# Kernel optimization log

Measured on AMD Instinct MI355X. Metric: run time of the kernel, lower is better.

## Reference

```python
import jax, jax.numpy as jnp
import numpy as np

N_DET, N_T, NY, NX, B = 128, 2048, 256, 256, 4


def setup_inputs() -> dict:
    key = jax.random.key(0)
    k1, k2, k3 = jax.random.split(key, 3)
    sino = jax.random.normal(k1, (B, 1, N_DET, N_T), dtype=jnp.float32)
    # lut[..., 0]: fractional time-of-flight index in [0, n_t-1)
    tof = jax.random.uniform(k2, (NY, NX, N_DET), dtype=jnp.float32) * (N_T - 1)
    # lut[..., 1]: linear-interp fraction alpha in [0, 1)
    alpha = jax.random.uniform(k3, (NY, NX, N_DET), dtype=jnp.float32)
    lut = jnp.stack([tof, alpha], axis=-1)  # [ny, nx, n_det, 2]
    return {"sino": sino, "lut": lut}


def reference(sino, lut):
    b, _, n_det, n_t = sino.shape
    ny, nx = lut.shape[0], lut.shape[1]
    P = ny * nx

    # Precompute (as in __init__): floor index, validity mask, interp fraction.
    k_floor = jnp.floor(lut[..., 0])
    valid = (k_floor >= 0) & (k_floor < n_t - 1)
    k0 = jnp.clip(k_floor, 0, max(n_t - 2, 0)).astype(jnp.int32)  # [ny,nx,n_det]
    alpha = lut[..., 1]

    # Hann apodization window over detectors (non-trainable buffer).
    apod = (0.5 - 0.5 * jnp.cos(
        2.0 * jnp.pi * jnp.arange(n_det, dtype=jnp.float32) / max(n_det - 1, 1)
    )).astype(sino.dtype)

    S = sino[:, 0]  # [B, n_det, n_t]

    # Move detector axis first so we can gather all detectors at once.
    k0t = k0.reshape(P, n_det).T          # [n_det, P]
    at = alpha.reshape(P, n_det).T        # [n_det, P]
    vt = valid.reshape(P, n_det).T.astype(sino.dtype)  # [n_det, P]

    s0 = jnp.take_along_axis(S, k0t[None], axis=2)        # [B, n_det, P]
    s1 = jnp.take_along_axis(S, (k0t + 1)[None], axis=2)  # [B, n_det, P]
    sk = ((1.0 - at) * s0 + at * s1) * vt                  # masked lerp

    out = jnp.einsum('d,bdp->bp', apod, sk)                # apodized reduce over detectors
    norm = jnp.maximum(apod.sum(), jnp.finfo(apod.dtype).tiny)
    return (out / norm).reshape(b, 1, ny, nx)
```

## Files before the change

### kernel.cpp

```cpp
#include <hip/hip_runtime.h>
#include <hip/hip_fp16.h>

#define N_DET 128
#define N_T   2048
#define NPIX  65536
#define NBATCH 4
#define G 8
#define PT 1024
#define NGB (N_DET / G)

typedef float f4_t __attribute__((ext_vector_type(4)));

__global__ __launch_bounds__(256) void sino_pack_kernel(
    const float* __restrict__ sino, float2* __restrict__ ws,
    float* __restrict__ out) {
  const int idx = blockIdx.x * blockDim.x + threadIdx.x;
  const __half2 lo = __floats2half2_rn(
      __builtin_nontemporal_load(sino + 0 * N_DET * N_T + idx),
      __builtin_nontemporal_load(sino + 1 * N_DET * N_T + idx));
  const __half2 hi = __floats2half2_rn(
      __builtin_nontemporal_load(sino + 2 * N_DET * N_T + idx),
      __builtin_nontemporal_load(sino + 3 * N_DET * N_T + idx));
  union { struct { __half2 a, b; } h; float2 f; } u;
  u.h.a = lo;
  u.h.b = hi;
  ws[idx] = u.f;
  out[idx] = 0.0f;
}

__global__ __launch_bounds__(1024, 4) void das_lds_kernel(
    const float* __restrict__ lut, const float2* __restrict__ ws,
    float* __restrict__ out) {
  __shared__ float2 sino_s[G * N_T];

  const int tid = threadIdx.x;
  const int tile = blockIdx.x;
  const int g = blockIdx.y;
  const int p = tile * PT + tid;

  f4_t l[4];
  {
    const f4_t* lp =
        reinterpret_cast<const f4_t*>(lut + ((size_t)p * N_DET + g * G) * 2);
#pragma unroll
    for (int j = 0; j < 4; ++j) l[j] = lp[j];
  }

  {
    const float4* src = reinterpret_cast<const float4*>(ws + (size_t)g * G * N_T);
    float4* dst = reinterpret_cast<float4*>(sino_s);
#pragma unroll
    for (int i = 0; i < 8192 / PT; ++i) dst[tid + i * PT] = src[tid + i * PT];
  }

  float apd[G];
#pragma unroll
  for (int j = 0; j < G; ++j) {
    apd[j] = 0.5f - 0.5f * cosf(6.28318530717958647692f *
                                ((float)(g * G + j) / (float)(N_DET - 1)));
  }
  __syncthreads();

  float a0 = 0.f, a1 = 0.f, a2 = 0.f, a3 = 0.f;
#pragma unroll
  for (int j = 0; j < G; ++j) {
    const float tof = (j & 1) ? l[j >> 1].z : l[j >> 1].x;
    const float al  = (j & 1) ? l[j >> 1].w : l[j >> 1].y;
    const float kf = floorf(tof);
    const bool valid = (kf >= 0.0f) && (kf < (float)(N_T - 1));
    const float kcl = fminf(fmaxf(kf, 0.0f), (float)(N_T - 2));
    const int k0 = (int)kcl;
    const float w = valid ? apd[j] : 0.0f;

    const float2 r0 = sino_s[j * N_T + k0];
    const float2 r1 = sino_s[j * N_T + k0 + 1];
    const __half2* h0 = reinterpret_cast<const __half2*>(&r0);
    const __half2* h1 = reinterpret_cast<const __half2*>(&r1);
    const float2 s0a = __half22float2(h0[0]);
    const float2 s0b = __half22float2(h0[1]);
    const float2 s1a = __half22float2(h1[0]);
    const float2 s1b = __half22float2(h1[1]);

    a0 += w * (s0a.x + al * (s1a.x - s0a.x));
    a1 += w * (s0a.y + al * (s1a.y - s0a.y));
    a2 += w * (s0b.x + al * (s1b.x - s0b.x));
    a3 += w * (s0b.y + al * (s1b.y - s0b.y));
  }
  const float nrm = 1.0f / 63.5f;
  atomicAdd(out + 0 * NPIX + p, a0 * nrm);
  atomicAdd(out + 1 * NPIX + p, a1 * nrm);
  atomicAdd(out + 2 * NPIX + p, a2 * nrm);
  atomicAdd(out + 3 * NPIX + p, a3 * nrm);
}

__global__ __launch_bounds__(256) void das_fallback_kernel(
    const float* __restrict__ lut, const float* __restrict__ S,
    float* __restrict__ out) {
  const int lane = threadIdx.x & 63;
  const int p = blockIdx.x * 4 + (threadIdx.x >> 6);

  const float4 lv =
      reinterpret_cast<const float4*>(lut + (size_t)p * 2 * N_DET)[lane];

  float acc0 = 0.f, acc1 = 0.f, acc2 = 0.f, acc3 = 0.f;
  float wsum = 0.f;

#pragma unroll
  for (int j = 0; j < 2; ++j) {
    const int d = 2 * lane + j;
    const float tof = j ? lv.z : lv.x;
    const float a   = j ? lv.w : lv.y;
    const float kf = floorf(tof);
    const bool valid = (kf >= 0.0f) && (kf < (float)(N_T - 1));
    const float kcl = fminf(fmaxf(kf, 0.0f), (float)(N_T - 2));
    const int k0 = (int)kcl;
    const float apd =
        0.5f - 0.5f * cosf(6.28318530717958647692f *
                           (1.0f / (float)(N_DET - 1)) * (float)d);
    wsum += apd;
    const float w = valid ? apd : 0.0f;
    const float om = 1.0f - a;
    const float* row = S + (size_t)d * N_T + k0;
    acc0 += w * (om * row[0 * N_DET * N_T] + a * row[0 * N_DET * N_T + 1]);
    acc1 += w * (om * row[1 * N_DET * N_T] + a * row[1 * N_DET * N_T + 1]);
    acc2 += w * (om * row[2 * N_DET * N_T] + a * row[2 * N_DET * N_T + 1]);
    acc3 += w * (om * row[3 * N_DET * N_T] + a * row[3 * N_DET * N_T + 1]);
  }

#pragma unroll
  for (int off = 32; off > 0; off >>= 1) {
    acc0 += __shfl_xor(acc0, off);
    acc1 += __shfl_xor(acc1, off);
    acc2 += __shfl_xor(acc2, off);
    acc3 += __shfl_xor(acc3, off);
    wsum += __shfl_xor(wsum, off);
  }

  if (lane == 0) {
    const float inv = 1.0f / fmaxf(wsum, 1.17549435e-38f);
    out[0 * NPIX + p] = acc0 * inv;
    out[1 * NPIX + p] = acc1 * inv;
    out[2 * NPIX + p] = acc2 * inv;
    out[3 * NPIX + p] = acc3 * inv;
  }
}

extern "C" void kernel_launch(void* const* d_in, const int* in_sizes, int n_in,
                              void* d_out, int out_size, void* d_ws, size_t ws_size,
                              hipStream_t stream) {
  const float* sino = (const float*)d_in[0];
  const float* lut  = (const float*)d_in[1];
  float* out = (float*)d_out;

  const size_t need = (size_t)N_DET * N_T * 8;
  if (ws_size >= need) {
    float2* ws = (float2*)d_ws;
    sino_pack_kernel<<<(N_DET * N_T) / 256, 256, 0, stream>>>(sino, ws, out);
    dim3 grid(NPIX / PT, NGB);
    das_lds_kernel<<<grid, 1024, 0, stream>>>(lut, ws, out);
  } else {
    das_fallback_kernel<<<NPIX / 4, 256, 0, stream>>>(lut, sino, out);
  }
}
```

Measured before the change: 122.7 us.

## Double-buffer sinogram LDS staging in 2-detector groups to overlap loads with compute

Each block now stages only two detector rows at a time into a double-buffered LDS array (64 KB instead of 128 KB), prefetching the next group from global memory into registers while it computes on the current group. The aim is to cut LDS footprint so more blocks can be resident per CU (launch bounds raised to 8) and to hide global-load latency behind the interpolation math. In exchange it adds four __syncthreads per block and recomputes the apodization cosine inline. Higher occupancy may be limited by registers at 1024 threads.

```diff
diff --git a/kernel.cpp b/kernel.cpp
--- a/kernel.cpp
+++ b/kernel.cpp
@@ -5,9 +5,11 @@
 #define N_T   2048
 #define NPIX  65536
 #define NBATCH 4
-#define G 8
+#define CHUNK 8
+#define NCHUNK (N_DET / CHUNK)
+#define G 2
+#define NGRP (CHUNK / G)
 #define PT 1024
-#define NGB (N_DET / G)
 
 typedef float f4_t __attribute__((ext_vector_type(4)));
 
@@ -28,64 +30,83 @@
   out[idx] = 0.0f;
 }
 
-__global__ __launch_bounds__(1024, 4) void das_lds_kernel(
+__global__ __launch_bounds__(1024, 8) void das_lds_kernel(
     const float* __restrict__ lut, const float2* __restrict__ ws,
     float* __restrict__ out) {
-  __shared__ float2 sino_s[G * N_T];
+  __shared__ float2 sino_s[2][G * N_T];
 
   const int tid = threadIdx.x;
   const int tile = blockIdx.x;
-  const int g = blockIdx.y;
+  const int c = blockIdx.y;
   const int p = tile * PT + tid;
 
   f4_t l[4];
   {
     const f4_t* lp =
-        reinterpret_cast<const f4_t*>(lut + ((size_t)p * N_DET + g * G) * 2);
+        reinterpret_cast<const f4_t*>(lut + ((size_t)p * N_DET + c * CHUNK) * 2);
 #pragma unroll
     for (int j = 0; j < 4; ++j) l[j] = lp[j];
   }
 
+  const float4* wsrc = reinterpret_cast<const float4*>(ws + (size_t)c * CHUNK * N_T);
   {
-    const float4* src = reinterpret_cast<const float4*>(ws + (size_t)g * G * N_T);
-    float4* dst = reinterpret_cast<float4*>(sino_s);
-#pragma unroll
-    for (int i = 0; i < 8192 / PT; ++i) dst[tid + i * PT] = src[tid + i * PT];
-  }
-
-  float apd[G];
-#pragma unroll
-  for (int j = 0; j < G; ++j) {
-    apd[j] = 0.5f - 0.5f * cosf(6.28318530717958647692f *
-                                ((float)(g * G + j) / (float)(N_DET - 1)));
+    const float4 s0 = wsrc[tid];
+    const float4 s1 = wsrc[tid + 1024];
+    float4* dst = reinterpret_cast<float4*>(&sino_s[0][0]);
+    dst[tid] = s0;
+    dst[tid + 1024] = s1;
   }
   __syncthreads();
 
   float a0 = 0.f, a1 = 0.f, a2 = 0.f, a3 = 0.f;
+
 #pragma unroll
-  for (int j = 0; j < G; ++j) {
-    const float tof = (j & 1) ? l[j >> 1].z : l[j >> 1].x;
-    const float al  = (j & 1) ? l[j >> 1].w : l[j >> 1].y;
-    const float kf = floorf(tof);
-    const bool valid = (kf >= 0.0f) && (kf < (float)(N_T - 1));
-    const float kcl = fminf(fmaxf(kf, 0.0f), (float)(N_T - 2));
-    const int k0 = (int)kcl;
-    const float w = valid ? apd[j] : 0.0f;
+  for (int grp = 0; grp < NGRP; ++grp) {
+    const int cur = grp & 1;
 
-    const float2 r0 = sino_s[j * N_T + k0];
-    const float2 r1 = sino_s[j * N_T + k0 + 1];
-    const __half2* h0 = reinterpret_cast<const __half2*>(&r0);
-    const __half2* h1 = reinterpret_cast<const __half2*>(&r1);
-    const float2 s0a = __half22float2(h0[0]);
-    const float2 s0b = __half22float2(h0[1]);
-    const float2 s1a = __half22float2(h1[0]);
-    const float2 s1b = __half22float2(h1[1]);
+    float4 n0, n1;
+    if (grp < NGRP - 1) {
+      n0 = wsrc[(grp + 1) * 2048 + tid];
+      n1 = wsrc[(grp + 1) * 2048 + tid + 1024];
+    }
 
-    a0 += w * (s0a.x + al * (s1a.x - s0a.x));
-    a1 += w * (s0a.y + al * (s1a.y - s0a.y));
-    a2 += w * (s0b.x + al * (s1b.x - s0b.x));
-    a3 += w * (s0b.y + al * (s1b.y - s0b.y));
+    const float2* sbuf = &sino_s[cur][0];
+#pragma unroll
+    for (int r = 0; r < G; ++r) {
+      const int d = c * CHUNK + grp * G + r;
+      const float tof = r ? l[grp].z : l[grp].x;
+      const float al  = r ? l[grp].w : l[grp].y;
+      const float kf = floorf(tof);
+      const bool valid = (kf >= 0.0f) && (kf < (float)(N_T - 1));
+      const float kcl = fminf(fmaxf(kf, 0.0f), (float)(N_T - 2));
+      const int k0 = (int)kcl;
+      const float apd = 0.5f - 0.5f * cosf(6.28318530717958647692f *
+                                           ((float)d / (float)(N_DET - 1)));
+      const float w = valid ? apd : 0.0f;
+
+      const float2 r0 = sbuf[r * N_T + k0];
+      const float2 r1 = sbuf[r * N_T + k0 + 1];
+      const __half2* h0 = reinterpret_cast<const __half2*>(&r0);
+      const __half2* h1 = reinterpret_cast<const __half2*>(&r1);
+      const float2 s0a = __half22float2(h0[0]);
+      const float2 s0b = __half22float2(h0[1]);
+      const float2 s1a = __half22float2(h1[0]);
+      const float2 s1b = __half22float2(h1[1]);
+
+      a0 += w * (s0a.x + al * (s1a.x - s0a.x));
+      a1 += w * (s0a.y + al * (s1a.y - s0a.y));
+      a2 += w * (s0b.x + al * (s1b.x - s0b.x));
+      a3 += w * (s0b.y + al * (s1b.y - s0b.y));
+    }
+
+    if (grp < NGRP - 1) {
+      float4* dst = reinterpret_cast<float4*>(&sino_s[cur ^ 1][0]);
+      dst[tid] = n0;
+      dst[tid + 1024] = n1;
+    }
+    __syncthreads();
   }
+
   const float nrm = 1.0f / 63.5f;
   atomicAdd(out + 0 * NPIX + p, a0 * nrm);
   atomicAdd(out + 1 * NPIX + p, a1 * nrm);
@@ -156,7 +177,7 @@
   if (ws_size >= need) {
     float2* ws = (float2*)d_ws;
     sino_pack_kernel<<<(N_DET * N_T) / 256, 256, 0, stream>>>(sino, ws, out);
-    dim3 grid(NPIX / PT, NGB);
+    dim3 grid(NPIX / PT, NCHUNK);
     das_lds_kernel<<<grid, 1024, 0, stream>>>(lut, ws, out);
   } else {
     das_fallback_kernel<<<NPIX / 4, 256, 0, stream>>>(lut, sino, out);
```

Result: slower. 137.8 us (+12.3%).

## Stream all detectors per block with double-buffered async LDS loads, drop atomics

Applied to the files above, without the earlier changes.

Each block now covers 256 pixels and loops over all 128 detectors in 32 iterations of 4 detectors, four threads per pixel. Packed sinogram rows are double-buffered into LDS with global_load_lds, so the next stage's copy overlaps the current gather. Partial sums are reduced with shuffles and written directly, which removes the atomics and the output zeroing in the pack kernel. The cost is a __syncthreads per iteration and each block re-reading the whole 2 MB packed sinogram (256 blocks instead of 1024 blocks each reading 128 KB), which raises L2 traffic.

```diff
diff --git a/kernel.cpp b/kernel.cpp
--- a/kernel.cpp
+++ b/kernel.cpp
@@ -5,15 +5,12 @@
 #define N_T   2048
 #define NPIX  65536
 #define NBATCH 4
-#define G 8
-#define PT 1024
-#define NGB (N_DET / G)
+#define PT 256
 
 typedef float f4_t __attribute__((ext_vector_type(4)));
 
 __global__ __launch_bounds__(256) void sino_pack_kernel(
-    const float* __restrict__ sino, float2* __restrict__ ws,
-    float* __restrict__ out) {
+    const float* __restrict__ sino, float2* __restrict__ ws) {
   const int idx = blockIdx.x * blockDim.x + threadIdx.x;
   const __half2 lo = __floats2half2_rn(
       __builtin_nontemporal_load(sino + 0 * N_DET * N_T + idx),
@@ -25,55 +22,67 @@
   u.h.a = lo;
   u.h.b = hi;
   ws[idx] = u.f;
-  out[idx] = 0.0f;
 }
 
 __global__ __launch_bounds__(1024, 4) void das_lds_kernel(
     const float* __restrict__ lut, const float2* __restrict__ ws,
     float* __restrict__ out) {
-  __shared__ float2 sino_s[G * N_T];
+  __shared__ __align__(16) float2 sbuf[2][4][N_T];
+  __shared__ float apod_s[N_DET];
 
   const int tid = threadIdx.x;
-  const int tile = blockIdx.x;
-  const int g = blockIdx.y;
-  const int p = tile * PT + tid;
+  const int pix = tid >> 2, sub = tid & 3;
+  const int p = blockIdx.x * PT + pix;
 
-  f4_t l[4];
-  {
-    const f4_t* lp =
-        reinterpret_cast<const f4_t*>(lut + ((size_t)p * N_DET + g * G) * 2);
+  if (tid < N_DET)
+    apod_s[tid] =
+        0.5f - 0.5f * cosf(6.28318530717958647692f * ((float)tid / 127.0f));
+
+  const f4_t* lp =
+      reinterpret_cast<const f4_t*>(lut + ((size_t)p * N_DET + sub * 32) * 2);
+  f4_t l[16];
+  l[0] = lp[0];
+
+  const int w = tid >> 6, lane = tid & 63;
+  const int q = w >> 2, sw = w & 3;
+  const char* gbase = reinterpret_cast<const char*>(ws) + ((size_t)q << 19) +
+                      (sw << 10) + lane * 16;
+  char* lbase = reinterpret_cast<char*>(&sbuf[0][0][0]) + (q << 14) +
+                (sw << 10) + lane * 16;
+
+  auto stage = [&](int it, int b) {
 #pragma unroll
-    for (int j = 0; j < 4; ++j) l[j] = lp[j];
-  }
+    for (int rr = 0; rr < 4; ++rr) {
+      __builtin_amdgcn_global_load_lds(
+          (const __attribute__((address_space(1))) void*)(gbase +
+                                                          ((size_t)it << 14) +
+                                                          (rr << 12)),
+          (__attribute__((address_space(3))) void*)(lbase + (b << 16) +
+                                                    (rr << 12)),
+          16, 0, 0);
+    }
+  };
 
-  {
-    const float4* src = reinterpret_cast<const float4*>(ws + (size_t)g * G * N_T);
-    float4* dst = reinterpret_cast<float4*>(sino_s);
-#pragma unroll
-    for (int i = 0; i < 8192 / PT; ++i) dst[tid + i * PT] = src[tid + i * PT];
-  }
-
-  float apd[G];
-#pragma unroll
-  for (int j = 0; j < G; ++j) {
-    apd[j] = 0.5f - 0.5f * cosf(6.28318530717958647692f *
-                                ((float)(g * G + j) / (float)(N_DET - 1)));
-  }
+  stage(0, 0);
   __syncthreads();
 
   float a0 = 0.f, a1 = 0.f, a2 = 0.f, a3 = 0.f;
+
 #pragma unroll
-  for (int j = 0; j < G; ++j) {
-    const float tof = (j & 1) ? l[j >> 1].z : l[j >> 1].x;
-    const float al  = (j & 1) ? l[j >> 1].w : l[j >> 1].y;
+  for (int it = 0; it < 32; ++it) {
+    if (it + 1 < 32) stage(it + 1, (it + 1) & 1);
+    if ((it & 1) == 1 && (it + 1) < 32) l[(it + 1) >> 1] = lp[(it + 1) >> 1];
+
+    const float tof = (it & 1) ? l[it >> 1].z : l[it >> 1].x;
+    const float al  = (it & 1) ? l[it >> 1].w : l[it >> 1].y;
     const float kf = floorf(tof);
     const bool valid = (kf >= 0.0f) && (kf < (float)(N_T - 1));
-    const float kcl = fminf(fmaxf(kf, 0.0f), (float)(N_T - 2));
-    const int k0 = (int)kcl;
-    const float w = valid ? apd[j] : 0.0f;
+    const int k0 = (int)fminf(fmaxf(kf, 0.0f), (float)(N_T - 2));
+    const float wgt = valid ? apod_s[sub * 32 + it] : 0.0f;
 
-    const float2 r0 = sino_s[j * N_T + k0];
-    const float2 r1 = sino_s[j * N_T + k0 + 1];
+    const float2* sb = &sbuf[it & 1][sub][0];
+    const float2 r0 = sb[k0];
+    const float2 r1 = sb[k0 + 1];
     const __half2* h0 = reinterpret_cast<const __half2*>(&r0);
     const __half2* h1 = reinterpret_cast<const __half2*>(&r1);
     const float2 s0a = __half22float2(h0[0]);
@@ -81,16 +90,26 @@
     const float2 s1a = __half22float2(h1[0]);
     const float2 s1b = __half22float2(h1[1]);
 
-    a0 += w * (s0a.x + al * (s1a.x - s0a.x));
-    a1 += w * (s0a.y + al * (s1a.y - s0a.y));
-    a2 += w * (s0b.x + al * (s1b.x - s0b.x));
-    a3 += w * (s0b.y + al * (s1b.y - s0b.y));
+    a0 += wgt * (s0a.x + al * (s1a.x - s0a.x));
+    a1 += wgt * (s0a.y + al * (s1a.y - s0a.y));
+    a2 += wgt * (s0b.x + al * (s1b.x - s0b.x));
+    a3 += wgt * (s0b.y + al * (s1b.y - s0b.y));
+
+    __syncthreads();
   }
-  const float nrm = 1.0f / 63.5f;
-  atomicAdd(out + 0 * NPIX + p, a0 * nrm);
-  atomicAdd(out + 1 * NPIX + p, a1 * nrm);
-  atomicAdd(out + 2 * NPIX + p, a2 * nrm);
-  atomicAdd(out + 3 * NPIX + p, a3 * nrm);
+
+  a0 += __shfl_xor(a0, 1); a0 += __shfl_xor(a0, 2);
+  a1 += __shfl_xor(a1, 1); a1 += __shfl_xor(a1, 2);
+  a2 += __shfl_xor(a2, 1); a2 += __shfl_xor(a2, 2);
+  a3 += __shfl_xor(a3, 1); a3 += __shfl_xor(a3, 2);
+
+  if (sub == 0) {
+    const float nrm = 1.0f / 63.5f;
+    out[0 * NPIX + p] = a0 * nrm;
+    out[1 * NPIX + p] = a1 * nrm;
+    out[2 * NPIX + p] = a2 * nrm;
+    out[3 * NPIX + p] = a3 * nrm;
+  }
 }
 
 __global__ __launch_bounds__(256) void das_fallback_kernel(
@@ -155,9 +174,8 @@
   const size_t need = (size_t)N_DET * N_T * 8;
   if (ws_size >= need) {
     float2* ws = (float2*)d_ws;
-    sino_pack_kernel<<<(N_DET * N_T) / 256, 256, 0, stream>>>(sino, ws, out);
-    dim3 grid(NPIX / PT, NGB);
-    das_lds_kernel<<<grid, 1024, 0, stream>>>(lut, ws, out);
+    sino_pack_kernel<<<(N_DET * N_T) / 256, 256, 0, stream>>>(sino, ws);
+    das_lds_kernel<<<NPIX / PT, 1024, 0, stream>>>(lut, ws, out);
   } else {
     das_fallback_kernel<<<NPIX / 4, 256, 0, stream>>>(lut, sino, out);
   }
```

Measured after the change: 229.8 us. +87.2%, slower.

## Replace LDS-staged detector groups with direct global gathers and warp-shuffle reduction

Applied to the files above, without the earlier changes.

The kernel no longer stages 8-detector slices of the packed sinogram into LDS and no longer reduces with global atomics. Each pixel is now handled by 16 lanes, each covering 8 detectors. Samples are gathered straight from the packed half-precision workspace, with one 16-byte load fetching both interpolation taps, and the partial sums are combined by shuffles and written once. This removes the LDS fill traffic, the atomics and the zeroing of the output, but relies on the L2/MALL cache to absorb random gathers over the whole 2 MB packed sinogram.

```diff
diff --git a/kernel.cpp b/kernel.cpp
--- a/kernel.cpp
+++ b/kernel.cpp
@@ -5,15 +5,14 @@
 #define N_T   2048
 #define NPIX  65536
 #define NBATCH 4
-#define G 8
-#define PT 1024
-#define NGB (N_DET / G)
+#define SUBS 16
+#define DPS (N_DET / SUBS)
 
 typedef float f4_t __attribute__((ext_vector_type(4)));
+typedef float f4u_t __attribute__((ext_vector_type(4), aligned(8)));
 
 __global__ __launch_bounds__(256) void sino_pack_kernel(
-    const float* __restrict__ sino, float2* __restrict__ ws,
-    float* __restrict__ out) {
+    const float* __restrict__ sino, float2* __restrict__ ws) {
   const int idx = blockIdx.x * blockDim.x + threadIdx.x;
   const __half2 lo = __floats2half2_rn(
       __builtin_nontemporal_load(sino + 0 * N_DET * N_T + idx),
@@ -25,72 +24,70 @@
   u.h.a = lo;
   u.h.b = hi;
   ws[idx] = u.f;
-  out[idx] = 0.0f;
 }
 
-__global__ __launch_bounds__(1024, 4) void das_lds_kernel(
-    const float* __restrict__ lut, const float2* __restrict__ ws,
+__global__ __launch_bounds__(256, 8) void das_gather_kernel(
+    const float* __restrict__ lut, const char* __restrict__ wsb,
     float* __restrict__ out) {
-  __shared__ float2 sino_s[G * N_T];
+  __shared__ float apod_s[N_DET];
 
   const int tid = threadIdx.x;
-  const int tile = blockIdx.x;
-  const int g = blockIdx.y;
-  const int p = tile * PT + tid;
+  if (tid < N_DET)
+    apod_s[tid] =
+        0.5f - 0.5f * cosf(6.28318530717958647692f * ((float)tid / 127.0f));
 
-  f4_t l[4];
-  {
-    const f4_t* lp =
-        reinterpret_cast<const f4_t*>(lut + ((size_t)p * N_DET + g * G) * 2);
+  const int sub = tid & (SUBS - 1);
+  const int p = (blockIdx.x * 256 + tid) >> 4;
+
+  const f4_t* lp =
+      reinterpret_cast<const f4_t*>(lut + ((size_t)p * N_DET + sub * DPS) * 2);
+  f4_t l[DPS / 2];
 #pragma unroll
-    for (int j = 0; j < 4; ++j) l[j] = lp[j];
-  }
+  for (int i = 0; i < DPS / 2; ++i) l[i] = lp[i];
 
-  {
-    const float4* src = reinterpret_cast<const float4*>(ws + (size_t)g * G * N_T);
-    float4* dst = reinterpret_cast<float4*>(sino_s);
-#pragma unroll
-    for (int i = 0; i < 8192 / PT; ++i) dst[tid + i * PT] = src[tid + i * PT];
-  }
-
-  float apd[G];
-#pragma unroll
-  for (int j = 0; j < G; ++j) {
-    apd[j] = 0.5f - 0.5f * cosf(6.28318530717958647692f *
-                                ((float)(g * G + j) / (float)(N_DET - 1)));
-  }
   __syncthreads();
 
   float a0 = 0.f, a1 = 0.f, a2 = 0.f, a3 = 0.f;
+  const unsigned rowbase = (unsigned)(sub * DPS) * (N_T * 8u);
+
 #pragma unroll
-  for (int j = 0; j < G; ++j) {
+  for (int j = 0; j < DPS; ++j) {
     const float tof = (j & 1) ? l[j >> 1].z : l[j >> 1].x;
     const float al  = (j & 1) ? l[j >> 1].w : l[j >> 1].y;
     const float kf = floorf(tof);
     const bool valid = (kf >= 0.0f) && (kf < (float)(N_T - 1));
-    const float kcl = fminf(fmaxf(kf, 0.0f), (float)(N_T - 2));
-    const int k0 = (int)kcl;
-    const float w = valid ? apd[j] : 0.0f;
+    const int k0 = (int)fminf(fmaxf(kf, 0.0f), (float)(N_T - 2));
+    const float w = valid ? apod_s[sub * DPS + j] : 0.0f;
 
-    const float2 r0 = sino_s[j * N_T + k0];
-    const float2 r1 = sino_s[j * N_T + k0 + 1];
-    const __half2* h0 = reinterpret_cast<const __half2*>(&r0);
-    const __half2* h1 = reinterpret_cast<const __half2*>(&r1);
-    const float2 s0a = __half22float2(h0[0]);
-    const float2 s0b = __half22float2(h0[1]);
-    const float2 s1a = __half22float2(h1[0]);
-    const float2 s1b = __half22float2(h1[1]);
+    const f4u_t g = *reinterpret_cast<const f4u_t*>(
+        wsb + rowbase + (unsigned)(j * N_T * 8) + ((unsigned)k0 << 3));
+    const __half2* h = reinterpret_cast<const __half2*>(&g);
+    const float2 s0a = __half22float2(h[0]);
+    const float2 s0b = __half22float2(h[1]);
+    const float2 s1a = __half22float2(h[2]);
+    const float2 s1b = __half22float2(h[3]);
 
     a0 += w * (s0a.x + al * (s1a.x - s0a.x));
     a1 += w * (s0a.y + al * (s1a.y - s0a.y));
     a2 += w * (s0b.x + al * (s1b.x - s0b.x));
     a3 += w * (s0b.y + al * (s1b.y - s0b.y));
   }
-  const float nrm = 1.0f / 63.5f;
-  atomicAdd(out + 0 * NPIX + p, a0 * nrm);
-  atomicAdd(out + 1 * NPIX + p, a1 * nrm);
-  atomicAdd(out + 2 * NPIX + p, a2 * nrm);
-  atomicAdd(out + 3 * NPIX + p, a3 * nrm);
+
+#pragma unroll
+  for (int off = 1; off < SUBS; off <<= 1) {
+    a0 += __shfl_xor(a0, off);
+    a1 += __shfl_xor(a1, off);
+    a2 += __shfl_xor(a2, off);
+    a3 += __shfl_xor(a3, off);
+  }
+
+  if (sub == 0) {
+    const float nrm = 1.0f / 63.5f;
+    out[0 * NPIX + p] = a0 * nrm;
+    out[1 * NPIX + p] = a1 * nrm;
+    out[2 * NPIX + p] = a2 * nrm;
+    out[3 * NPIX + p] = a3 * nrm;
+  }
 }
 
 __global__ __launch_bounds__(256) void das_fallback_kernel(
@@ -155,9 +152,9 @@
   const size_t need = (size_t)N_DET * N_T * 8;
   if (ws_size >= need) {
     float2* ws = (float2*)d_ws;
-    sino_pack_kernel<<<(N_DET * N_T) / 256, 256, 0, stream>>>(sino, ws, out);
-    dim3 grid(NPIX / PT, NGB);
-    das_lds_kernel<<<grid, 1024, 0, stream>>>(lut, ws, out);
+    sino_pack_kernel<<<(N_DET * N_T) / 256, 256, 0, stream>>>(sino, ws);
+    das_gather_kernel<<<(NPIX * SUBS) / 256, 256, 0, stream>>>(
+        lut, (const char*)ws, out);
   } else {
     das_fallback_kernel<<<NPIX / 4, 256, 0, stream>>>(lut, sino, out);
   }
```

Result: slower. 126.0 us (+2.7%).
